# Optimization experiments

Hardware: AMD Instinct MI355X
Metric: run time of the kernel (lower is better)

The kernel has to match this reference:

```python
import jax, jax.numpy as jnp
import numpy as np

B, CIN, COUT, H, W, K, WDIM = 16, 512, 512, 32, 32, 3, 512


def setup_inputs() -> dict:
    key = jax.random.key(0)
    k0, k1, k2, k3 = jax.random.split(key, 4)
    return {
        "image": jax.random.normal(k0, (B, CIN, H, W), dtype=jnp.float32),
        "w_latent": jax.random.normal(k1, (B, WDIM), dtype=jnp.float32),
        "dense_kernel": jax.random.normal(k2, (WDIM, CIN), dtype=jnp.float32) * 0.02,
        "dense_bias": jnp.zeros((CIN,), dtype=jnp.float32),
        "conv_weights": jax.random.normal(k3, (K, K, CIN, COUT), dtype=jnp.float32),
    }


def reference(image, w_latent, dense_kernel, dense_bias, conv_weights):
    # style scale from Dense(w) -> [B, Cin]
    style = w_latent @ dense_kernel + dense_bias
    # per-sample modulated weights: [B, kh, kw, Cin, Cout]
    w = conv_weights[None] * style[:, None, None, :, None]
    # faithful to source: reduce over axes [2,3,4] (kw, Cin, Cout) -> [B, kh];
    # no epsilon added (source defines but never uses self.epsilon)
    denom = jax.lax.rsqrt(jnp.sum(w * w, axis=(2, 3, 4)))
    w = w * denom[:, :, None, None, None]
    b, cin, h, wid = image.shape
    cout = w.shape[-1]
    # batch-as-groups trick: [1, B*Cin, H, W] conv [kh, kw, Cin, B*Cout] with groups=B
    eff_img = image.reshape(1, b * cin, h, wid)
    eff_filt = jnp.transpose(w, (1, 2, 3, 0, 4)).reshape(w.shape[1], w.shape[2], cin, b * cout)
    out = jax.lax.conv_general_dilated(
        eff_img, eff_filt,
        window_strides=(1, 1), padding="SAME",
        dimension_numbers=("NCHW", "HWIO", "NCHW"),
        feature_group_count=b,
    )
    return out.reshape(b, cout, out.shape[2], out.shape[3])
```

## Files before the change

### kernel.cpp

```cpp
#include <hip/hip_runtime.h>
#include <hip/hip_bf16.h>


typedef short short8 __attribute__((ext_vector_type(8)));
typedef float f32x4 __attribute__((ext_vector_type(4)));

__device__ __forceinline__ ushort bf16_rtne(float f) {
    unsigned u = __float_as_uint(f);
    unsigned r = u + 0x7fffu + ((u >> 16) & 1u);
    return (ushort)(r >> 16);
}
__device__ __forceinline__ float bf16_up(ushort h) {
    return __uint_as_float(((unsigned)h) << 16);
}
__device__ __forceinline__ void gld16(const void* g, void* l) {
    __builtin_amdgcn_global_load_lds(
        (const __attribute__((address_space(1))) unsigned int*)g,
        (__attribute__((address_space(3))) unsigned int*)l, 16, 0, 0);
}

__global__ __launch_bounds__(256) void style_kernel(const float* __restrict__ wl,
                                                    const float* __restrict__ dk,
                                                    const float* __restrict__ bias,
                                                    float* __restrict__ style) {
    __shared__ float wsh[512];
    __shared__ float red[4][64];
    const int b = blockIdx.y, c0 = blockIdx.x * 64, t = threadIdx.x;
    for (int i = t; i < 512; i += 256) wsh[i] = wl[b * 512 + i];
    __syncthreads();
    const int c = c0 + (t & 63), kq = (t >> 6) * 128;
    float acc = 0.f;
    #pragma unroll 8
    for (int k = 0; k < 128; ++k)
        acc = fmaf(wsh[kq + k], dk[(size_t)(kq + k) * 512 + c], acc);
    red[t >> 6][t & 63] = acc;
    __syncthreads();
    if (t < 64)
        style[b * 512 + c0 + t] =
            red[0][t] + red[1][t] + red[2][t] + red[3][t] + bias[c0 + t];
}

__global__ void wsum_kernel(const float* __restrict__ cw, float* __restrict__ S) {
    int bid = blockIdx.x;
    int kh = bid >> 9, cin = bid & 511;
    int lane = threadIdx.x;
    float acc = 0.f;
    #pragma unroll
    for (int kw = 0; kw < 3; ++kw) {
        const float* p = cw + ((size_t)((kh * 3 + kw) << 9) + cin) * 512;
        for (int co = lane; co < 512; co += 64) {
            float v = p[co];
            acc = fmaf(v, v, acc);
        }
    }
    #pragma unroll
    for (int off = 32; off; off >>= 1) acc += __shfl_down(acc, off);
    if (lane == 0) S[bid] = acc;
}

__global__ void denom_kernel(const float* __restrict__ S,
                             const float* __restrict__ style,
                             float* __restrict__ dn) {
    int bid = blockIdx.x;
    int b = bid / 3, kh = bid % 3;
    int lane = threadIdx.x;
    float acc = 0.f;
    for (int c = lane; c < 512; c += 64) {
        float s = style[b * 512 + c];
        acc = fmaf(S[kh * 512 + c], s * s, acc);
    }
    #pragma unroll
    for (int off = 32; off; off >>= 1) acc += __shfl_down(acc, off);
    if (lane == 0) dn[bid] = rsqrtf(acc);
}

__global__ __launch_bounds__(256) void wsplit_kernel(const float* __restrict__ cw,
                                                     ushort* __restrict__ wthi,
                                                     ushort* __restrict__ wtlo) {
    __shared__ ushort hs[64][72];
    __shared__ ushort ls[64][72];
    int t = threadIdx.x;
    int k0 = blockIdx.x * 64, c0 = blockIdx.y * 64;
    int col = t & 63;
    int rq = t >> 6;
    #pragma unroll
    for (int i = 0; i < 16; ++i) {
        int kr = rq * 16 + i;
        float v = cw[(size_t)(k0 + kr) * 512 + c0 + col];
        ushort hh = bf16_rtne(v);
        ushort ll = bf16_rtne(v - bf16_up(hh));
        hs[col][kr] = hh;
        ls[col][kr] = ll;
    }
    __syncthreads();
    int r = t >> 2, kq = (t & 3) << 4;
    int cout = c0 + r;
    int k = k0 + kq;
    size_t o = ((size_t)(cout >> 7) * 144 + (k >> 5)) * 4096 +
               (size_t)(cout & 127) * 32 + (k & 31);
    *(uint4*)&wthi[o]     = *(const uint4*)&hs[r][kq];
    *(uint4*)&wthi[o + 8] = *(const uint4*)&hs[r][kq + 8];
    *(uint4*)&wtlo[o]     = *(const uint4*)&ls[r][kq];
    *(uint4*)&wtlo[o + 8] = *(const uint4*)&ls[r][kq + 8];
}

__global__ __launch_bounds__(256) void isplit_kernel(const float* __restrict__ img,
                                                     const float* __restrict__ style,
                                                     ushort* __restrict__ ihi,
                                                     ushort* __restrict__ ilo) {
    const int b = blockIdx.y, yp = blockIdx.x, t = threadIdx.x;
    const size_t rowbase = (size_t)(b * 34 + yp) * 34 * 512;
    uint4 z = {0u, 0u, 0u, 0u};
    if (yp == 0 || yp == 33) {
        for (int i = t; i < 2176; i += 256) {
            ((uint4*)(ihi + rowbase))[i] = z;
            ((uint4*)(ilo + rowbase))[i] = z;
        }
        return;
    }
    if (t < 64) {
        ((uint4*)(ihi + rowbase))[t] = z;
        ((uint4*)(ilo + rowbase))[t] = z;
        ((uint4*)(ihi + rowbase + 33 * 512))[t] = z;
        ((uint4*)(ilo + rowbase + 33 * 512))[t] = z;
    }
    const int y = yp - 1;
    __shared__ float buf[64][33];
    const int ci = t >> 5, x = t & 31;
    const int xo = t >> 3, cs = (t & 7) * 8;
    for (int c0 = 0; c0 < 512; c0 += 64) {
        __syncthreads();
        #pragma unroll
        for (int i = 0; i < 8; ++i) {
            int cin = c0 + ci + i * 8;
            float v = img[((size_t)(b * 512 + cin) * 32 + y) * 32 + x] *
                      style[b * 512 + cin];
            buf[ci + i * 8][x] = v;
        }
        __syncthreads();
        union { ushort u[8]; uint4 v; } hb, lb;
        #pragma unroll
        for (int i = 0; i < 8; ++i) {
            float v = buf[cs + i][xo];
            ushort hh = bf16_rtne(v);
            hb.u[i] = hh;
            lb.u[i] = bf16_rtne(v - bf16_up(hh));
        }
        size_t o = rowbase + (size_t)(xo + 1) * 512 + c0 + cs;
        *(uint4*)&ihi[o] = hb.v;
        *(uint4*)&ilo[o] = lb.v;
    }
}

__global__ __launch_bounds__(256) void conv_gemm(
    const ushort* __restrict__ wt2hi,
    const ushort* __restrict__ wt2lo,
    const ushort* __restrict__ ihi,
    const ushort* __restrict__ ilo,
    const float*  __restrict__ dn,
    float* __restrict__ out)
{
    __shared__ ushort Wh[128][32];
    __shared__ ushort Wo[128][32];
    __shared__ ushort Ih[128][32];
    __shared__ ushort Io[128][32];

    const int tid  = threadIdx.x;
    const int lane = tid & 63;
    const int wid  = tid >> 6;

    const int pixblk  = blockIdx.x;
    const int coutblk = blockIdx.y;
    const int b         = pixblk >> 3;
    const int pix_base  = (pixblk & 7) << 7;
    const int wr = (wid >> 1) * 64;
    const int wc = (wid & 1) * 64;
    const int rl = lane & 15;
    const int kg = (lane >> 4) << 3;

    const int r0 = wid << 5;
    const int rA = r0 + (lane >> 2);
    const int rB = rA + 16;
    const int ck = (lane & 3) << 3;

    const size_t wcb = (size_t)coutblk * 144 * 4096;
    const ushort* wAh = wt2hi + wcb + rA * 32 + ck;
    const ushort* wBh = wt2hi + wcb + rB * 32 + ck;
    const ushort* wAl = wt2lo + wcb + rA * 32 + ck;
    const ushort* wBl = wt2lo + wcb + rB * 32 + ck;

    const size_t ibase = (size_t)b * 34 * 34 * 512;
    const int gpA = pix_base + rA, gpB = pix_base + rB;
    const int pAoff = ((gpA >> 5) * 34 + (gpA & 31)) * 512 + ck;
    const int pBoff = ((gpB >> 5) * 34 + (gpB & 31)) * 512 + ck;
    const ushort* iAh = ihi + ibase + pAoff;
    const ushort* iBh = ihi + ibase + pBoff;
    const ushort* iAl = ilo + ibase + pAoff;
    const ushort* iBl = ilo + ibase + pBoff;

    ushort* lWhA = &Wh[r0][0];      ushort* lWhB = &Wh[r0 + 16][0];
    ushort* lWoA = &Wo[r0][0];      ushort* lWoB = &Wo[r0 + 16][0];
    ushort* lIhA = &Ih[r0][0];      ushort* lIhB = &Ih[r0 + 16][0];
    ushort* lIoA = &Io[r0][0];      ushort* lIoB = &Io[r0 + 16][0];

    const float d0 = dn[b * 3 + 0];
    const float d1 = dn[b * 3 + 1];
    const float d2 = dn[b * 3 + 2];

    f32x4 acc[4][4];
    #pragma unroll
    for (int i = 0; i < 4; ++i)
        #pragma unroll
        for (int j = 0; j < 4; ++j) acc[i][j] = (f32x4)0.f;

    int step = 0;
    for (int seg = 0; seg < 3; ++seg) {
        for (int s = 0; s < 48; ++s, ++step) {
            const int k0  = step << 5;
            const int khw = k0 >> 9;
            const int kh  = khw >= 6 ? 2 : (khw >= 3 ? 1 : 0);
            const int kw  = khw - kh * 3;
            const int soff = (kh * 34 + kw) * 512 + (k0 & 511);
            const int wst  = step << 12;

            __syncthreads();
            gld16(wAh + wst, lWhA);
            gld16(wBh + wst, lWhB);
            gld16(wAl + wst, lWoA);
            gld16(wBl + wst, lWoB);
            gld16(iAh + soff, lIhA);
            gld16(iBh + soff, lIhB);
            gld16(iAl + soff, lIoA);
            gld16(iBl + soff, lIoB);
            __syncthreads();

            short8 wa[4], wl8[4], ia[4], il8[4];
            #pragma unroll
            for (int mi = 0; mi < 4; ++mi) {
                wa[mi]  = *(const short8*)&Wh[wr + mi * 16 + rl][kg];
                wl8[mi] = *(const short8*)&Wo[wr + mi * 16 + rl][kg];
            }
            #pragma unroll
            for (int ni = 0; ni < 4; ++ni) {
                ia[ni]  = *(const short8*)&Ih[wc + ni * 16 + rl][kg];
                il8[ni] = *(const short8*)&Io[wc + ni * 16 + rl][kg];
            }
            #pragma unroll
            for (int mi = 0; mi < 4; ++mi)
                #pragma unroll
                for (int ni = 0; ni < 4; ++ni) {
                    acc[mi][ni] = __builtin_amdgcn_mfma_f32_16x16x32_bf16(
                        wa[mi], ia[ni], acc[mi][ni], 0, 0, 0);
                    acc[mi][ni] = __builtin_amdgcn_mfma_f32_16x16x32_bf16(
                        wa[mi], il8[ni], acc[mi][ni], 0, 0, 0);
                    acc[mi][ni] = __builtin_amdgcn_mfma_f32_16x16x32_bf16(
                        wl8[mi], ia[ni], acc[mi][ni], 0, 0, 0);
                }
        }
        if (seg < 2) {
            const float rr = (seg == 0) ? (d0 / d1) : (d1 / d2);
            #pragma unroll
            for (int mi = 0; mi < 4; ++mi)
                #pragma unroll
                for (int ni = 0; ni < 4; ++ni) acc[mi][ni] *= rr;
        }
    }

    const int cout_base = coutblk << 7;
    #pragma unroll
    for (int mi = 0; mi < 4; ++mi) {
        const int crow = cout_base + wr + mi * 16 + ((lane >> 4) << 2);
        #pragma unroll
        for (int ni = 0; ni < 4; ++ni) {
            const int ccol = pix_base + wc + ni * 16 + (lane & 15);
            float* op = out + ((size_t)(b << 9) + crow) * 1024 + ccol;
            f32x4 c = acc[mi][ni];
            #pragma unroll
            for (int r = 0; r < 4; ++r)
                op[(size_t)r * 1024] = c[r] * d2;
        }
    }
}

extern "C" void kernel_launch(void* const* d_in, const int* in_sizes, int n_in,
                              void* d_out, int out_size, void* d_ws, size_t ws_size,
                              hipStream_t stream) {
    const float* img  = (const float*)d_in[0];
    const float* wl   = (const float*)d_in[1];
    const float* dk   = (const float*)d_in[2];
    const float* bias = (const float*)d_in[3];
    const float* cw   = (const float*)d_in[4];
    float* out = (float*)d_out;

    float* style = (float*)d_ws;
    float* S     = style + 8192;
    float* dn    = S + 1536;
    ushort* wt2hi = (ushort*)((char*)d_ws + 65536);
    ushort* wt2lo = wt2hi + (size_t)4 * 144 * 4096;
    ushort* ihi   = wt2lo + (size_t)4 * 144 * 4096;
    ushort* ilo   = ihi   + (size_t)16 * 34 * 34 * 512;

    style_kernel<<<dim3(8, 16), 256, 0, stream>>>(wl, dk, bias, style);
    wsum_kernel<<<1536, 64, 0, stream>>>(cw, S);
    denom_kernel<<<48, 64, 0, stream>>>(S, style, dn);
    wsplit_kernel<<<dim3(72, 8), 256, 0, stream>>>(cw, wt2hi, wt2lo);
    isplit_kernel<<<dim3(34, 16), 256, 0, stream>>>(img, style, ihi, ilo);

    conv_gemm<<<dim3(128, 4), 256, 0, stream>>>(wt2hi, wt2lo, ihi, ilo, dn, out);
}
```

Baseline: 329.6 us.

## Double-buffer image tiles, stream weights via registers, swizzle LDS, fuse weight norms

The conv GEMM now loads weight fragments straight into registers, using a pre-packed MFMA-fragment layout and a ping-pong register prefetch. Image tiles are double-buffered in LDS with an XOR swizzle, so only one barrier is needed per K-step and bank conflicts are reduced. The squared-weight sums are fused into the weight-split kernel using atomics, which removes a separate pass over the conv weights, and blocks are remapped so neighbouring blocks share weight tiles. The costs are higher register pressure from the 16 prefetched short8 values, floating-point atomics whose summation order is nondeterministic, and an extra memset.

```diff
diff --git a/kernel.cpp b/kernel.cpp
--- a/kernel.cpp
+++ b/kernel.cpp
@@ -40,24 +40,6 @@
             red[0][t] + red[1][t] + red[2][t] + red[3][t] + bias[c0 + t];
 }
 
-__global__ void wsum_kernel(const float* __restrict__ cw, float* __restrict__ S) {
-    int bid = blockIdx.x;
-    int kh = bid >> 9, cin = bid & 511;
-    int lane = threadIdx.x;
-    float acc = 0.f;
-    #pragma unroll
-    for (int kw = 0; kw < 3; ++kw) {
-        const float* p = cw + ((size_t)((kh * 3 + kw) << 9) + cin) * 512;
-        for (int co = lane; co < 512; co += 64) {
-            float v = p[co];
-            acc = fmaf(v, v, acc);
-        }
-    }
-    #pragma unroll
-    for (int off = 32; off; off >>= 1) acc += __shfl_down(acc, off);
-    if (lane == 0) S[bid] = acc;
-}
-
 __global__ void denom_kernel(const float* __restrict__ S,
                              const float* __restrict__ style,
                              float* __restrict__ dn) {
@@ -75,14 +57,16 @@
 }
 
 __global__ __launch_bounds__(256) void wsplit_kernel(const float* __restrict__ cw,
-                                                     ushort* __restrict__ wthi,
-                                                     ushort* __restrict__ wtlo) {
+                                                     ushort* __restrict__ wt3,
+                                                     float* __restrict__ S) {
     __shared__ ushort hs[64][72];
     __shared__ ushort ls[64][72];
     int t = threadIdx.x;
     int k0 = blockIdx.x * 64, c0 = blockIdx.y * 64;
     int col = t & 63;
     int rq = t >> 6;
+    const int khw = k0 >> 9;
+    const int kh = khw >= 6 ? 2 : (khw >= 3 ? 1 : 0);
     #pragma unroll
     for (int i = 0; i < 16; ++i) {
         int kr = rq * 16 + i;
@@ -91,17 +75,23 @@
         ushort ll = bf16_rtne(v - bf16_up(hh));
         hs[col][kr] = hh;
         ls[col][kr] = ll;
+        float sq = v * v;
+        #pragma unroll
+        for (int off = 32; off; off >>= 1) sq += __shfl_down(sq, off);
+        if ((t & 63) == 0)
+            atomicAdd(&S[kh * 512 + ((k0 & 511) + kr)], sq);
     }
     __syncthreads();
     int r = t >> 2, kq = (t & 3) << 4;
     int cout = c0 + r;
     int k = k0 + kq;
-    size_t o = ((size_t)(cout >> 7) * 144 + (k >> 5)) * 4096 +
-               (size_t)(cout & 127) * 32 + (k & 31);
-    *(uint4*)&wthi[o]     = *(const uint4*)&hs[r][kq];
-    *(uint4*)&wthi[o + 8] = *(const uint4*)&hs[r][kq + 8];
-    *(uint4*)&wtlo[o]     = *(const uint4*)&ls[r][kq];
-    *(uint4*)&wtlo[o + 8] = *(const uint4*)&ls[r][kq + 8];
+    size_t o = ((size_t)((cout >> 7) * 144 + (k >> 5)) * 2 + ((cout >> 6) & 1)) * 4096
+             + (size_t)((cout >> 4) & 3) * 1024
+             + (size_t)(((k >> 3) & 3) * 16 + (cout & 15)) * 8;
+    *(uint4*)&wt3[o]       = *(const uint4*)&hs[r][kq];
+    *(uint4*)&wt3[o + 128] = *(const uint4*)&hs[r][kq + 8];
+    *(uint4*)&wt3[o + 512] = *(const uint4*)&ls[r][kq];
+    *(uint4*)&wt3[o + 640] = *(const uint4*)&ls[r][kq + 8];
 }
 
 __global__ __launch_bounds__(256) void isplit_kernel(const float* __restrict__ img,
@@ -128,6 +118,10 @@
     __shared__ float buf[64][33];
     const int ci = t >> 5, x = t & 31;
     const int xo = t >> 3, cs = (t & 7) * 8;
+    const int xp = xo + 1;
+    const int sig = (xp >> 1) & 3;
+    const size_t o_sw = rowbase + (size_t)xp * 512 + (cs & 32)
+                      + (size_t)((((cs >> 3) & 3) ^ sig) << 3);
     for (int c0 = 0; c0 < 512; c0 += 64) {
         __syncthreads();
         #pragma unroll
@@ -146,62 +140,48 @@
             hb.u[i] = hh;
             lb.u[i] = bf16_rtne(v - bf16_up(hh));
         }
-        size_t o = rowbase + (size_t)(xo + 1) * 512 + c0 + cs;
-        *(uint4*)&ihi[o] = hb.v;
-        *(uint4*)&ilo[o] = lb.v;
-    }
-}
-
-__global__ __launch_bounds__(256) void conv_gemm(
-    const ushort* __restrict__ wt2hi,
-    const ushort* __restrict__ wt2lo,
-    const ushort* __restrict__ ihi,
-    const ushort* __restrict__ ilo,
+        *(uint4*)&ihi[o_sw + c0] = hb.v;
+        *(uint4*)&ilo[o_sw + c0] = lb.v;
+    }
+}
+
+__global__ __launch_bounds__(256, 2) void conv_gemm(
+    const ushort* __restrict__ wt3,
+    const ushort* __restrict__ ihh,
+    const ushort* __restrict__ ihl,
     const float*  __restrict__ dn,
     float* __restrict__ out)
 {
-    __shared__ ushort Wh[128][32];
-    __shared__ ushort Wo[128][32];
-    __shared__ ushort Ih[128][32];
-    __shared__ ushort Io[128][32];
+    __shared__ ushort Ih[2][128][32];
+    __shared__ ushort Io[2][128][32];
 
     const int tid  = threadIdx.x;
     const int lane = tid & 63;
     const int wid  = tid >> 6;
 
-    const int pixblk  = blockIdx.x;
-    const int coutblk = blockIdx.y;
-    const int b         = pixblk >> 3;
-    const int pix_base  = (pixblk & 7) << 7;
+    const int g   = blockIdx.x;
+    const int swz = ((g & 7) << 6) | (g >> 3);
+    const int coutblk = swz >> 7;
+    const int pixblk  = swz & 127;
+    const int b        = pixblk >> 3;
+    const int pix_base = (pixblk & 7) << 7;
+
     const int wr = (wid >> 1) * 64;
     const int wc = (wid & 1) * 64;
-    const int rl = lane & 15;
-    const int kg = (lane >> 4) << 3;
+    const int rl  = lane & 15;
+    const int kgB = (lane >> 4) << 3;
 
     const int r0 = wid << 5;
     const int rA = r0 + (lane >> 2);
     const int rB = rA + 16;
     const int ck = (lane & 3) << 3;
-
-    const size_t wcb = (size_t)coutblk * 144 * 4096;
-    const ushort* wAh = wt2hi + wcb + rA * 32 + ck;
-    const ushort* wBh = wt2hi + wcb + rB * 32 + ck;
-    const ushort* wAl = wt2lo + wcb + rA * 32 + ck;
-    const ushort* wBl = wt2lo + wcb + rB * 32 + ck;
-
     const size_t ibase = (size_t)b * 34 * 34 * 512;
     const int gpA = pix_base + rA, gpB = pix_base + rB;
-    const int pAoff = ((gpA >> 5) * 34 + (gpA & 31)) * 512 + ck;
-    const int pBoff = ((gpB >> 5) * 34 + (gpB & 31)) * 512 + ck;
-    const ushort* iAh = ihi + ibase + pAoff;
-    const ushort* iBh = ihi + ibase + pBoff;
-    const ushort* iAl = ilo + ibase + pAoff;
-    const ushort* iBl = ilo + ibase + pBoff;
-
-    ushort* lWhA = &Wh[r0][0];      ushort* lWhB = &Wh[r0 + 16][0];
-    ushort* lWoA = &Wo[r0][0];      ushort* lWoB = &Wo[r0 + 16][0];
-    ushort* lIhA = &Ih[r0][0];      ushort* lIhB = &Ih[r0 + 16][0];
-    ushort* lIoA = &Io[r0][0];      ushort* lIoB = &Io[r0 + 16][0];
+    const size_t pAoff = ibase + (size_t)((gpA >> 5) * 34 + (gpA & 31)) * 512 + ck;
+    const size_t pBoff = ibase + (size_t)((gpB >> 5) * 34 + (gpB & 31)) * 512 + ck;
+
+    const int half = wid >> 1;
+    const ushort* wpBase = wt3 + (size_t)coutblk * 1179648 + (size_t)half * 4096 + lane * 8;
 
     const float d0 = dn[b * 3 + 0];
     const float d1 = dn[b * 3 + 1];
@@ -213,58 +193,72 @@
         #pragma unroll
         for (int j = 0; j < 4; ++j) acc[i][j] = (f32x4)0.f;
 
-    int step = 0;
-    for (int seg = 0; seg < 3; ++seg) {
-        for (int s = 0; s < 48; ++s, ++step) {
-            const int k0  = step << 5;
-            const int khw = k0 >> 9;
-            const int kh  = khw >= 6 ? 2 : (khw >= 3 ? 1 : 0);
-            const int kw  = khw - kh * 3;
-            const int soff = (kh * 34 + kw) * 512 + (k0 & 511);
-            const int wst  = step << 12;
-
-            __syncthreads();
-            gld16(wAh + wst, lWhA);
-            gld16(wBh + wst, lWhB);
-            gld16(wAl + wst, lWoA);
-            gld16(wBl + wst, lWoB);
-            gld16(iAh + soff, lIhA);
-            gld16(iBh + soff, lIhB);
-            gld16(iAl + soff, lIoA);
-            gld16(iBl + soff, lIoB);
-            __syncthreads();
-
-            short8 wa[4], wl8[4], ia[4], il8[4];
-            #pragma unroll
-            for (int mi = 0; mi < 4; ++mi) {
-                wa[mi]  = *(const short8*)&Wh[wr + mi * 16 + rl][kg];
-                wl8[mi] = *(const short8*)&Wo[wr + mi * 16 + rl][kg];
-            }
-            #pragma unroll
-            for (int ni = 0; ni < 4; ++ni) {
-                ia[ni]  = *(const short8*)&Ih[wc + ni * 16 + rl][kg];
-                il8[ni] = *(const short8*)&Io[wc + ni * 16 + rl][kg];
-            }
-            #pragma unroll
-            for (int mi = 0; mi < 4; ++mi)
-                #pragma unroll
-                for (int ni = 0; ni < 4; ++ni) {
-                    acc[mi][ni] = __builtin_amdgcn_mfma_f32_16x16x32_bf16(
-                        wa[mi], ia[ni], acc[mi][ni], 0, 0, 0);
-                    acc[mi][ni] = __builtin_amdgcn_mfma_f32_16x16x32_bf16(
-                        wa[mi], il8[ni], acc[mi][ni], 0, 0, 0);
-                    acc[mi][ni] = __builtin_amdgcn_mfma_f32_16x16x32_bf16(
-                        wl8[mi], ia[ni], acc[mi][ni], 0, 0, 0);
-                }
-        }
-        if (seg < 2) {
-            const float rr = (seg == 0) ? (d0 / d1) : (d1 / d2);
-            #pragma unroll
-            for (int mi = 0; mi < 4; ++mi)
-                #pragma unroll
-                for (int ni = 0; ni < 4; ++ni) acc[mi][ni] *= rr;
-        }
-    }
+    short8 wRegA[8], wRegB[8];
+
+    gld16(ihh + pAoff, &Ih[0][r0][0]);
+    gld16(ihh + pBoff, &Ih[0][r0 + 16][0]);
+    gld16(ihl + pAoff, &Io[0][r0][0]);
+    gld16(ihl + pBoff, &Io[0][r0 + 16][0]);
+    #pragma unroll
+    for (int j = 0; j < 8; ++j) wRegA[j] = *(const short8*)(wpBase + j * 512);
+    __syncthreads();
+
+#define CONV_BODY(STEP, CUR, WUSE, WPRE)                                          \
+    {                                                                             \
+        const int step = (STEP);                                                  \
+        const int khw  = step >> 4;                                               \
+        const int kh   = khw >= 6 ? 2 : (khw >= 3 ? 1 : 0);                       \
+        const int kw   = khw - kh * 3;                                            \
+        if (step < 143) {                                                         \
+            const int s1   = step + 1;                                            \
+            const int khw1 = s1 >> 4;                                             \
+            const int kh1  = khw1 >= 6 ? 2 : (khw1 >= 3 ? 1 : 0);                 \
+            const int kw1  = khw1 - kh1 * 3;                                      \
+            const int soff1 = (kh1 * 34 + kw1) * 512 + ((s1 << 5) & 511);         \
+            gld16(ihh + pAoff + soff1, &Ih[(CUR) ^ 1][r0][0]);                    \
+            gld16(ihh + pBoff + soff1, &Ih[(CUR) ^ 1][r0 + 16][0]);               \
+            gld16(ihl + pAoff + soff1, &Io[(CUR) ^ 1][r0][0]);                    \
+            gld16(ihl + pBoff + soff1, &Io[(CUR) ^ 1][r0 + 16][0]);               \
+            const ushort* wsrc = wpBase + (size_t)s1 * 8192;                      \
+            _Pragma("unroll")                                                     \
+            for (int j = 0; j < 8; ++j) WPRE[j] = *(const short8*)(wsrc + j * 512);\
+        }                                                                         \
+        const int sig = (((rl + kw) >> 1) & 3) << 3;                              \
+        const int colr = kgB ^ sig;                                               \
+        short8 ia[4], il[4];                                                      \
+        _Pragma("unroll")                                                         \
+        for (int ni = 0; ni < 4; ++ni) {                                          \
+            const int row = wc + ni * 16 + rl;                                    \
+            ia[ni] = *(const short8*)&Ih[CUR][row][colr];                         \
+            il[ni] = *(const short8*)&Io[CUR][row][colr];                         \
+        }                                                                         \
+        _Pragma("unroll")                                                         \
+        for (int mi = 0; mi < 4; ++mi) {                                          \
+            _Pragma("unroll")                                                     \
+            for (int ni = 0; ni < 4; ++ni) {                                      \
+                acc[mi][ni] = __builtin_amdgcn_mfma_f32_16x16x32_bf16(            \
+                    WUSE[mi * 2 + 0], ia[ni], acc[mi][ni], 0, 0, 0);              \
+                acc[mi][ni] = __builtin_amdgcn_mfma_f32_16x16x32_bf16(            \
+                    WUSE[mi * 2 + 0], il[ni], acc[mi][ni], 0, 0, 0);              \
+                acc[mi][ni] = __builtin_amdgcn_mfma_f32_16x16x32_bf16(            \
+                    WUSE[mi * 2 + 1], ia[ni], acc[mi][ni], 0, 0, 0);              \
+            }                                                                     \
+        }                                                                         \
+        if (step == 47 || step == 95) {                                           \
+            const float rr = (step == 47) ? (d0 / d1) : (d1 / d2);                \
+            _Pragma("unroll")                                                     \
+            for (int mi = 0; mi < 4; ++mi)                                        \
+                _Pragma("unroll")                                                 \
+                for (int ni = 0; ni < 4; ++ni) acc[mi][ni] *= rr;                 \
+        }                                                                         \
+        __syncthreads();                                                          \
+    }
+
+    for (int it = 0; it < 72; ++it) {
+        CONV_BODY(2 * it,     0, wRegA, wRegB)
+        CONV_BODY(2 * it + 1, 1, wRegB, wRegA)
+    }
+#undef CONV_BODY
 
     const int cout_base = coutblk << 7;
     #pragma unroll
@@ -295,16 +289,15 @@
     float* style = (float*)d_ws;
     float* S     = style + 8192;
     float* dn    = S + 1536;
-    ushort* wt2hi = (ushort*)((char*)d_ws + 65536);
-    ushort* wt2lo = wt2hi + (size_t)4 * 144 * 4096;
-    ushort* ihi   = wt2lo + (size_t)4 * 144 * 4096;
-    ushort* ilo   = ihi   + (size_t)16 * 34 * 34 * 512;
-
+    ushort* wt3  = (ushort*)((char*)d_ws + 65536);
+    ushort* ihi  = wt3 + (size_t)4 * 144 * 8192;
+    ushort* ilo  = ihi + (size_t)16 * 34 * 34 * 512;
+
+    hipMemsetAsync(S, 0, 1536 * sizeof(float), stream);
     style_kernel<<<dim3(8, 16), 256, 0, stream>>>(wl, dk, bias, style);
-    wsum_kernel<<<1536, 64, 0, stream>>>(cw, S);
+    wsplit_kernel<<<dim3(72, 8), 256, 0, stream>>>(cw, wt3, S);
     denom_kernel<<<48, 64, 0, stream>>>(S, style, dn);
-    wsplit_kernel<<<dim3(72, 8), 256, 0, stream>>>(cw, wt2hi, wt2lo);
     isplit_kernel<<<dim3(34, 16), 256, 0, stream>>>(img, style, ihi, ilo);
 
-    conv_gemm<<<dim3(128, 4), 256, 0, stream>>>(wt2hi, wt2lo, ihi, ilo, dn, out);
-}
+    conv_gemm<<<512, 256, 0, stream>>>(wt3, ihi, ilo, dn, out);
+}
```

Measured after the change: 357.1 us. +8.3%, slower.
